# Optimization experiments

Measured on AMD Instinct MI355X. Metric: run time of the kernel, lower is better.

## Reference

```python
import jax, jax.numpy as jnp
import numpy as np

FS = 20.832e6      # sampling rate [Hz]
FDEMOD = 5.208e6   # demodulation frequency [Hz]
C = 1540.0         # sound speed [m/s]
FNUM = 1.0
MIN_W = 1e-3
EPS = 1e-5         # BatchNorm eps
EVENT = 0
TWO_PI = 2.0 * np.pi


def _cba(x, w, b, g, beta, pad):
    # Conv2d (NCHW) + BatchNorm2d (training-mode batch stats, biased var) + ReLU
    y = jax.lax.conv_general_dilated(x, w, (1, 1), ((0, 0), (pad, pad)),
                                     dimension_numbers=('NCHW', 'OIHW', 'NCHW'))
    y = y + b[None, :, None, None]
    mu = jnp.mean(y, axis=(0, 2, 3), keepdims=True)
    var = jnp.mean((y - mu) ** 2, axis=(0, 2, 3), keepdims=True)
    y = (y - mu) * jax.lax.rsqrt(var + EPS) * g[None, :, None, None] + beta[None, :, None, None]
    return jax.nn.relu(y)


def _forward(idata, qdata, angles, ele_pos, time_zero, grid,
             conv_w1, conv_b1, bn_g1, bn_b1,
             conv_w2, conv_b2, bn_g2, bn_b2,
             conv_w3, conv_b3, bn_g3, bn_b3,
             conv_w4, conv_b4, bn_g4, bn_b4):
    # --- normalization of raw I/Q data ---
    nrm = jnp.max(jnp.sqrt(idata ** 2 + qdata ** 2))
    idat = idata / nrm
    qdat = qdata / nrm
    H, Wd = grid.shape[:2]
    pix = grid.reshape(-1, 3)                               # [P,3]
    E = ele_pos.shape[0]
    ns = idat.shape[-1]
    ang = angles[EVENT]
    # --- delays in samples: plane-wave tx delay + per-element rx focus delay ---
    txdel = (pix[:, 0] * jnp.sin(ang) + pix[:, 2] * jnp.cos(ang)
             + time_zero[EVENT] * C) * (FS / C)             # [P]
    rxdel = jnp.linalg.norm(pix[None, :, :] - ele_pos[:, None, :], axis=-1) * (FS / C)  # [E,P]
    delays = txdel[None, :] + rxdel                         # [E,P]
    # --- 1D linear interp with zero padding ---
    # (grid_sample(bilinear, align_corners=False) on a 1xN image with the
    #  coordinate mapping in the source is exactly sampling at `delays`)
    d0 = jnp.floor(delays)
    frac = delays - d0
    d0i = d0.astype(jnp.int32)

    def gather(sig, idx):  # sig [E,ns], idx [E,P]
        v = jnp.take_along_axis(sig, jnp.clip(idx, 0, ns - 1), axis=1)
        return jnp.where((idx >= 0) & (idx < ns), v, 0.0)

    isig, qsig = idat[EVENT], qdat[EVENT]                   # [E,ns]
    ifoc = gather(isig, d0i) * (1.0 - frac) + gather(isig, d0i + 1) * frac
    qfoc = gather(qsig, d0i) * (1.0 - frac) + gather(qsig, d0i + 1) * frac
    # --- complex demodulation rotation ---
    tshift = delays / FS - pix[None, :, 2] * 2.0 / C
    theta = TWO_PI * FDEMOD * tshift
    ct, st = jnp.cos(theta), jnp.sin(theta)
    ir = ifoc * ct - qfoc * st
    qr = qfoc * ct + ifoc * st
    # [1,H,W,E,2]  (== torch idas/qdas view + squeeze(-2))
    inputData = jnp.transpose(jnp.stack([ir, qr], axis=-1), (1, 0, 2)).reshape(H, Wd, E, 2)[None]
    # --- receive apodization (orthogonal f-number mask), [H,W,E] ---
    v = pix[None, :, :] - ele_pos[:, None, :]
    vx, vz = v[:, :, 0], v[:, :, 2]
    px = pix[None, :, 0]
    # |vz/vx| > fnum written division-free as |vz| > fnum*|vx| (equivalent since vz>0)
    mrx = ((jnp.abs(vz) > FNUM * jnp.abs(vx)) | (jnp.abs(vx) <= MIN_W)
           | ((vx >= MIN_W) & (px <= ele_pos[0, 0]))
           | ((vx <= -MIN_W) & (px >= ele_pos[-1, 0])))
    apod_rx = jnp.transpose(mrx.astype(jnp.float32).reshape(E, H, Wd), (1, 2, 0))
    # --- transmit apodization (plane-wave footprint), [H,W] ---
    x_proj = pix[:, 0] - pix[:, 2] * jnp.tan(ang)
    mtx = (x_proj >= ele_pos[0, 0] * 1.2) & (x_proj <= ele_pos[-1, 0] * 1.2)
    apod_tx = mtx.astype(jnp.float32).reshape(H, Wd)
    inputData = inputData * apod_rx[None, :, :, :, None] * apod_tx[None, :, :, None, None]
    # --- per-element weighting CNN over [1, 2, H*W, E] ---
    x = jnp.transpose(inputData, (0, 4, 3, 1, 2)).reshape(1, 2, E, H * Wd)
    x = jnp.swapaxes(x, 2, 3)                               # [1,2,HW,E]
    x = _cba(x, conv_w1, conv_b1, bn_g1, bn_b1, 32)
    x = _cba(x, conv_w2, conv_b2, bn_g2, bn_b2, 7)
    x = _cba(x, conv_w3, conv_b3, bn_g3, bn_b3, 7)
    x = _cba(x, conv_w4, conv_b4, bn_g4, bn_b4, 1)          # [1,1,HW,E]
    weights = jnp.swapaxes(x[:, 0], 1, 2).reshape(1, E, H, Wd)
    singleW = jnp.sum(weights, axis=1)                      # [1,H,W]
    comp = jnp.mean(inputData * singleW[:, :, :, None, None], axis=-2)  # [1,H,W,2]
    mag = jnp.sqrt(jnp.sum(comp ** 2, axis=-1))
    ydb = 20.0 * jnp.log10(mag + 1e-20)
    y = ydb[0]
    return y - jnp.max(y)


def setup_inputs():
    key = jax.random.key(0)
    ks = jax.random.split(key, 8)
    na, ne, ns = 16, 128, 2048
    H, Wd = 128, 256
    idata = jax.random.normal(ks[0], (na, ne, ns), jnp.float32)
    qdata = jax.random.normal(ks[1], (na, ne, ns), jnp.float32)
    angles = jnp.linspace(-0.1, 0.1, na, dtype=jnp.float32)
    ex = jnp.linspace(-19.05e-3, 19.05e-3, ne, dtype=jnp.float32)
    ele_pos = jnp.stack([ex, jnp.zeros(ne, jnp.float32), jnp.zeros(ne, jnp.float32)], axis=-1)
    time_zero = jnp.zeros((na,), jnp.float32)
    xg = jnp.linspace(-17e-3, 17e-3, H, dtype=jnp.float32)
    zg = jnp.linspace(5e-3, 55e-3, Wd, dtype=jnp.float32)
    gx, gz = jnp.meshgrid(xg, zg, indexing='ij')
    grid = jnp.stack([gx, jnp.zeros_like(gx), gz], axis=-1)

    def conv_init(k, o, i, kh, kw):
        return jax.random.normal(k, (o, i, kh, kw), jnp.float32) * (1.0 / np.sqrt(i * kh * kw))

    return dict(idata=idata, qdata=qdata, angles=angles, ele_pos=ele_pos,
                time_zero=time_zero, grid=grid,
                conv_w1=conv_init(ks[2], 8, 2, 1, 65), conv_b1=jnp.zeros(8, jnp.float32),
                bn_g1=jnp.ones(8, jnp.float32), bn_b1=jnp.zeros(8, jnp.float32),
                conv_w2=conv_init(ks[3], 8, 8, 1, 15), conv_b2=jnp.zeros(8, jnp.float32),
                bn_g2=jnp.ones(8, jnp.float32), bn_b2=jnp.zeros(8, jnp.float32),
                conv_w3=conv_init(ks[4], 8, 8, 1, 15), conv_b3=jnp.zeros(8, jnp.float32),
                bn_g3=jnp.ones(8, jnp.float32), bn_b3=jnp.zeros(8, jnp.float32),
                conv_w4=conv_init(ks[5], 1, 8, 1, 3), conv_b4=jnp.zeros(1, jnp.float32),
                bn_g4=jnp.ones(1, jnp.float32), bn_b4=jnp.zeros(1, jnp.float32))


def reference(idata, qdata, angles, ele_pos, time_zero, grid,
              conv_w1, conv_b1, bn_g1, bn_b1,
              conv_w2, conv_b2, bn_g2, bn_b2,
              conv_w3, conv_b3, bn_g3, bn_b3,
              conv_w4, conv_b4, bn_g4, bn_b4):
    return _forward(idata, qdata, angles, ele_pos, time_zero, grid,
                    conv_w1, conv_b1, bn_g1, bn_b1,
                    conv_w2, conv_b2, bn_g2, bn_b2,
                    conv_w3, conv_b3, bn_g3, bn_b3,
                    conv_w4, conv_b4, bn_g4, bn_b4)
```

## Files before the change

### kernel.cpp

```cpp
#include <hip/hip_runtime.h>
#include <hip/hip_bf16.h>


#define E_    128
#define NPIX  32768
#define NS_   (NPIX * E_)
#define NSAMP 2048

static constexpr double PI_D     = 3.14159265358979323846;
static constexpr double FS_D     = 20832000.0;
static constexpr double FDEMOD_D = 5208000.0;
static constexpr double C_D      = 1540.0;

typedef __attribute__((ext_vector_type(8))) short short8;
typedef __attribute__((ext_vector_type(4))) float f32x4;

union U8 { uint4 u4; unsigned u32[4]; unsigned short us[8]; short8 s8; };

__device__ __forceinline__ unsigned short f2bf(float f) {
  unsigned u = __float_as_uint(f);
  unsigned r = (u + 0x7fffu + ((u >> 16) & 1u)) >> 16;
  return (unsigned short)r;
}
__device__ __forceinline__ unsigned cvt_pk_bf16(float lo, float hi) {
  unsigned r;
  asm("v_cvt_pk_bf16_f32 %0, %1, %2" : "=v"(r) : "v"(lo), "v"(hi));
  return r;
}
__device__ __forceinline__ float bflo(unsigned w) { return __uint_as_float(w << 16); }
__device__ __forceinline__ float bfhi(unsigned w) { return __uint_as_float(w & 0xFFFF0000u); }
__device__ __forceinline__ float bf2f(unsigned short s) {
  return __uint_as_float((unsigned)s << 16);
}

__device__ __forceinline__ float wave_reduce_sum(float v) {
  #pragma unroll
  for (int off = 32; off; off >>= 1) v += __shfl_xor(v, off);
  return v;
}
__device__ __forceinline__ float wave_reduce_max(float v) {
  #pragma unroll
  for (int off = 32; off; off >>= 1) v = fmaxf(v, __shfl_xor(v, off));
  return v;
}

template <int NBLK>
__device__ __forceinline__ void stats8v(const float4* __restrict__ part4,
                                        const float* __restrict__ g,
                                        const float* __restrict__ beta,
                                        float* __restrict__ A,
                                        float* __restrict__ Bc) {
  __shared__ float red[4][16];
  __shared__ float sums[16];
  const int tid = threadIdx.x;
  constexpr int K = (NBLK * 4) / 256;
  float ax = 0.f, ay = 0.f, az = 0.f, aw = 0.f;
  #pragma unroll
  for (int k = 0; k < K; ++k) {
    const float4 q = part4[tid + k * 256];
    ax += q.x; ay += q.y; az += q.z; aw += q.w;
  }
  #pragma unroll
  for (int off = 4; off <= 32; off <<= 1) {
    ax += __shfl_xor(ax, off);
    ay += __shfl_xor(ay, off);
    az += __shfl_xor(az, off);
    aw += __shfl_xor(aw, off);
  }
  const int lane = tid & 63, wv = tid >> 6;
  if (lane < 4) {
    red[wv][lane * 4 + 0] = ax;
    red[wv][lane * 4 + 1] = ay;
    red[wv][lane * 4 + 2] = az;
    red[wv][lane * 4 + 3] = aw;
  }
  __syncthreads();
  if (tid < 16)
    sums[tid] = red[0][tid] + red[1][tid] + red[2][tid] + red[3][tid];
  __syncthreads();
  if (tid < 8) {
    const float s = sums[tid], ss = sums[tid + 8];
    const float count = (float)NS_;
    const float mu = s / count;
    const float var = fmaxf(ss / count - mu * mu, 0.f);
    const float Av = g[tid] * rsqrtf(var + 1e-5f);
    red[0][tid] = Av;
    red[1][tid] = beta[tid] - mu * Av;
  }
  __syncthreads();
  #pragma unroll
  for (int i = 0; i < 8; ++i) { A[i] = red[0][i]; Bc[i] = red[1][i]; }
}

__device__ __forceinline__ uint4 bn_unit(uint4 v, const float* A, const float* B) {
  U8 in; in.u4 = v;
  unsigned ow[4];
  #pragma unroll
  for (int w = 0; w < 4; ++w) {
    const unsigned wd = in.u32[w];
    const float yl = fmaxf(0.f, fmaf(A[2 * w], bflo(wd), B[2 * w]));
    const float yh = fmaxf(0.f, fmaf(A[2 * w + 1], bfhi(wd), B[2 * w + 1]));
    ow[w] = cvt_pk_bf16(yl, yh);
  }
  return make_uint4(ow[0], ow[1], ow[2], ow[3]);
}

__global__ __launch_bounds__(256) void k_init(const float4* __restrict__ id4,
                                              const float4* __restrict__ qd4,
                                              float* __restrict__ pmaxsq) {
  const int idx = blockIdx.x * 256 + threadIdx.x;
  const float4 iv = id4[idx];
  const float4 qv = qd4[idx];
  float m = fmaxf(fmaxf(iv.x * iv.x + qv.x * qv.x, iv.y * iv.y + qv.y * qv.y),
                  fmaxf(iv.z * iv.z + qv.z * qv.z, iv.w * iv.w + qv.w * qv.w));
  m = wave_reduce_max(m);
  __shared__ float sm[4];
  if ((threadIdx.x & 63) == 0) sm[threadIdx.x >> 6] = m;
  __syncthreads();
  if (threadIdx.x == 0)
    pmaxsq[blockIdx.x] = fmaxf(fmaxf(sm[0], sm[1]), fmaxf(sm[2], sm[3]));
}

__global__ __launch_bounds__(256) void k_beamform(
    const float4* __restrict__ id4, const float4* __restrict__ qd4,
    const float* __restrict__ angles, const float* __restrict__ ele_pos,
    const float* __restrict__ time_zero, const float* __restrict__ grid,
    const float* __restrict__ pmaxsq, unsigned* __restrict__ x0t) {
  __shared__ float2 sig[NSAMP];
  __shared__ float smax[4];
  const int e = blockIdx.x & 127;
  const int chunk = blockIdx.x >> 7;

  const float4* irow = id4 + e * (NSAMP / 4);
  const float4* qrow = qd4 + e * (NSAMP / 4);
  #pragma unroll
  for (int k0 = 0; k0 < 2; ++k0) {
    const int k = k0 * 256 + threadIdx.x;
    const float4 iv = irow[k];
    const float4 qv = qrow[k];
    sig[4 * k + 0] = make_float2(iv.x, qv.x);
    sig[4 * k + 1] = make_float2(iv.y, qv.y);
    sig[4 * k + 2] = make_float2(iv.z, qv.z);
    sig[4 * k + 3] = make_float2(iv.w, qv.w);
  }
  float mx = 0.f;
  for (int i = threadIdx.x; i < 4096; i += 256) mx = fmaxf(mx, pmaxsq[i]);
  mx = wave_reduce_max(mx);
  if ((threadIdx.x & 63) == 0) smax[threadIdx.x >> 6] = mx;
  __syncthreads();
  const float inv =
      1.0f / sqrtf(fmaxf(fmaxf(smax[0], smax[1]), fmaxf(smax[2], smax[3])));

  const float ang = angles[0];
  const float tz  = time_zero[0];

  constexpr float SC    = (float)(FS_D / C_D);
  constexpr float TH2R  = (float)(2.0 * FDEMOD_D / C_D);
  constexpr float TWOPI = (float)(2.0 * PI_D);

  const float sa = __sinf(ang);
  const float ca = __cosf(ang);
  const float ta = sa / ca;
  const float ex  = ele_pos[e * 3];
  const float ex0 = ele_pos[0];
  const float exl = ele_pos[127 * 3];

  #pragma unroll
  for (int s = 0; s < 4; ++s) {
    const int p = chunk * 1024 + s * 256 + threadIdx.x;
    const float px = grid[p * 3 + 0];
    const float pz = grid[p * 3 + 2];

    const float txdel = (px * sa + pz * ca + tz * (float)C_D) * SC;
    const float dx = px - ex;
    const float rxdel = sqrtf(dx * dx + pz * pz) * SC;

    const float delays = txdel + rxdel;
    const float d0 = floorf(delays);
    const float frac = delays - d0;
    const int i0 = (int)d0;

    const int c0 = min(max(i0, 0), NSAMP - 1);
    const int c1 = min(max(i0 + 1, 0), NSAMP - 1);
    const float2 s0 = sig[c0];
    const float2 s1 = sig[c1];
    const bool m0 = (i0 >= 0) && (i0 < NSAMP);
    const bool m1 = (i0 + 1 >= 0) && (i0 + 1 < NSAMP);
    const float iv0 = m0 ? s0.x : 0.f;
    const float qv0 = m0 ? s0.y : 0.f;
    const float iv1 = m1 ? s1.x : 0.f;
    const float qv1 = m1 ? s1.y : 0.f;
    const float ifoc = (iv0 * (1.f - frac) + iv1 * frac) * inv;
    const float qfoc = (qv0 * (1.f - frac) + qv1 * frac) * inv;

    const float trev = fmaf(delays, 0.25f, -pz * TH2R);
    const float fr = trev - floorf(trev);
    const float st = __sinf(fr * TWOPI);
    const float ct = __cosf(fr * TWOPI);
    const float ir = ifoc * ct - qfoc * st;
    const float qr = qfoc * ct + ifoc * st;

    const float avx = fabsf(dx);
    const bool mrx = (fabsf(pz) > avx) || (avx <= 0.001f) ||
                     ((dx >= 0.001f) && (px <= ex0)) ||
                     ((dx <= -0.001f) && (px >= exl));
    const float xproj = px - pz * ta;
    const bool mtx = (xproj >= ex0 * 1.2f) && (xproj <= exl * 1.2f);
    const float a = (mrx && mtx) ? 1.f : 0.f;

    x0t[(size_t)e * NPIX + p] = cvt_pk_bf16(ir * a, qr * a);
  }
}

#define CONV1_P 32
#define ROWW    213

__global__ __launch_bounds__(256, 4) void k_conv1(
    const unsigned* __restrict__ x0t, const float* __restrict__ wgt,
    const float* __restrict__ bias, uint2* __restrict__ outp,
    float* __restrict__ partial,
    float* __restrict__ sumI, float* __restrict__ sumQ) {
  __shared__ unsigned tile[CONV1_P * ROWW];
  const int tid = threadIdx.x;
  const int lane = tid & 63;
  const int wv = tid >> 6;
  const int n = lane & 15, kq = lane >> 4;
  const int p0 = blockIdx.x * CONV1_P;

  short8 af2[6];
  #pragma unroll
  for (int m = 0; m < 6; ++m) {
    U8 u;
    #pragma unroll
    for (int j = 0; j < 8; ++j) {
      const int oc = n & 7;
      const int mm = (n < 8) ? m : (m - 1);
      const int tap = mm * 16 + kq * 4 + (j >> 1);
      const int ic = j & 1;
      const float w = (mm >= 0 && tap < 65) ? wgt[(oc * 2 + ic) * 65 + tap] : 0.f;
      u.us[j] = f2bf(w);
    }
    af2[m] = u.s8;
  }
  float bias_r[4];
  #pragma unroll
  for (int r = 0; r < 4; ++r) bias_r[r] = bias[(kq & 1) * 4 + r];

  for (int i = tid; i < CONV1_P * 32; i += 256)
    tile[(i >> 5) * ROWW + (i & 31)] = 0u;
  for (int i = tid; i < CONV1_P * 64; i += 256) {
    const int c = i & 63;
    if (c < ROWW - 160) tile[(i >> 6) * ROWW + 160 + c] = 0u;
  }
  {
    const int lp = tid & 31;
    const int e0 = tid >> 5;
    #pragma unroll
    for (int i = 0; i < 16; ++i) {
      const int e = i * 8 + e0;
      tile[lp * ROWW + 32 + e] = x0t[(size_t)e * NPIX + p0 + lp];
    }
  }
  __syncthreads();

  float sum[4] = {0, 0, 0, 0}, ssq[4] = {0, 0, 0, 0};
  const int sbase = n + kq * 4;

  for (int j8 = 0; j8 < 8; ++j8) {
    const int lpx = wv * 8 + j8;
    const int p = p0 + lpx;
    const unsigned* row = tile + lpx * ROWW;
    uint2* orow = outp + (size_t)p * 256;

    {
      const unsigned v0 = row[32 + lane];
      const unsigned v1 = row[96 + lane];
      float si = bflo(v0) + bflo(v1);
      float sq = bfhi(v0) + bfhi(v1);
      si = wave_reduce_sum(si);
      sq = wave_reduce_sum(sq);
      if (lane == 0) { sumI[p] = si; sumQ[p] = sq; }
    }

    U8 win[12];
    #pragma unroll
    for (int q = 0; q < 12; ++q)
      #pragma unroll
      for (int c = 0; c < 4; ++c) win[q].u32[c] = row[sbase + 16 * q + c];

    #pragma unroll
    for (int pi = 0; pi < 4; ++pi) {
      f32x4 acc = {bias_r[0], bias_r[1], bias_r[2], bias_r[3]};
      #pragma unroll
      for (int m = 0; m < 6; ++m)
        acc = __builtin_amdgcn_mfma_f32_16x16x32_bf16(af2[m], win[2 * pi + m].s8,
                                                      acc, 0, 0, 0);
      const unsigned lo = cvt_pk_bf16(acc[0], acc[1]);
      const unsigned hi = cvt_pk_bf16(acc[2], acc[3]);
      orow[((2 * pi + (kq >> 1)) * 16 + n) * 2 + (kq & 1)] = make_uint2(lo, hi);
      #pragma unroll
      for (int r = 0; r < 4; ++r) { const float v = acc[r]; sum[r] += v; ssq[r] += v * v; }
    }
  }

  #pragma unroll
  for (int off = 1; off <= 8; off <<= 1)
    #pragma unroll
    for (int r = 0; r < 4; ++r) { sum[r] += __shfl_xor(sum[r], off); ssq[r] += __shfl_xor(ssq[r], off); }
  #pragma unroll
  for (int r = 0; r < 4; ++r) { sum[r] += __shfl_xor(sum[r], 32); ssq[r] += __shfl_xor(ssq[r], 32); }
  __shared__ float s_red[4][16];
  if (lane == 0)
    #pragma unroll
    for (int r = 0; r < 4; ++r) { s_red[wv][r] = sum[r]; s_red[wv][8 + r] = ssq[r]; }
  if (lane == 16)
    #pragma unroll
    for (int r = 0; r < 4; ++r) { s_red[wv][4 + r] = sum[r]; s_red[wv][12 + r] = ssq[r]; }
  __syncthreads();
  if (tid < 16)
    partial[blockIdx.x * 16 + tid] =
        s_red[0][tid] + s_red[1][tid] + s_red[2][tid] + s_red[3][tid];
}

template <int NBLK_IN>
__global__ __launch_bounds__(256) void k_conv23(
    const uint4* __restrict__ inp, const float* __restrict__ wgt,
    const float* __restrict__ bias,
    const float4* __restrict__ part_in,
    const float* __restrict__ g_in, const float* __restrict__ be_in,
    uint2* __restrict__ outp, float* __restrict__ partial) {
  __shared__ uint4 s_row[4][144];
  const int tid = threadIdx.x;
  const int lane = tid & 63;
  const int wv = tid >> 6;
  const int gw = blockIdx.x * 4 + wv;
  const int n = lane & 15, kq = lane >> 4;

  uint4 v0 = inp[(size_t)gw * 128 + lane];
  uint4 v1 = inp[(size_t)gw * 128 + 64 + lane];

  float A[8], Bc[8];
  stats8v<NBLK_IN>(part_in, g_in, be_in, A, Bc);

  short8 af[4];
  #pragma unroll
  for (int m = 0; m < 4; ++m) {
    U8 u;
    #pragma unroll
    for (int j = 0; j < 8; ++j) {
      const int tap = m * 4 + kq;
      const float w = (n < 8 && tap < 15) ? wgt[(n * 8 + j) * 15 + tap] : 0.f;
      u.us[j] = f2bf(w);
    }
    af[m] = u.s8;
  }
  float bias_r[4];
  #pragma unroll
  for (int r = 0; r < 4; ++r) {
    const int oo = kq * 4 + r;
    bias_r[r] = (oo < 8) ? bias[oo] : 0.f;
  }

  uint4* lds = s_row[wv];
  if (lane < 7)  lds[lane] = make_uint4(0, 0, 0, 0);
  if (lane >= 7 && lane < 16) lds[128 + lane] = make_uint4(0, 0, 0, 0);

  float sum[4] = {0, 0, 0, 0}, ssq[4] = {0, 0, 0, 0};

  #pragma unroll 1
  for (int it = 0; it < 4; ++it) {
    const int p = gw + it * 8192;
    lds[7 + lane]  = bn_unit(v0, A, Bc);
    lds[71 + lane] = bn_unit(v1, A, Bc);

    if (it < 3) {
      const uint4* ng = inp + (size_t)(p + 8192) * 128;
      v0 = ng[lane];
      v1 = ng[64 + lane];
    }

    uint2* orow = outp + (size_t)p * 256;
    for (int t = 0; t < 8; ++t) {
      f32x4 acc = {bias_r[0], bias_r[1], bias_r[2], bias_r[3]};
      const int base = t * 16 + n + kq;
      #pragma unroll
      for (int m = 0; m < 4; ++m) {
        U8 b;
        b.u4 = lds[base + m * 4];
        acc = __builtin_amdgcn_mfma_f32_16x16x32_bf16(af[m], b.s8, acc, 0, 0, 0);
      }
      if (lane < 32) {
        const unsigned lo = cvt_pk_bf16(acc[0], acc[1]);
        const unsigned hi = cvt_pk_bf16(acc[2], acc[3]);
        orow[(t * 16 + n) * 2 + kq] = make_uint2(lo, hi);
        #pragma unroll
        for (int r = 0; r < 4; ++r) { const float v = acc[r]; sum[r] += v; ssq[r] += v * v; }
      }
    }
  }

  #pragma unroll
  for (int off = 1; off <= 8; off <<= 1)
    #pragma unroll
    for (int r = 0; r < 4; ++r) { sum[r] += __shfl_xor(sum[r], off); ssq[r] += __shfl_xor(ssq[r], off); }
  __shared__ float s_red[4][16];
  if (lane == 0)
    #pragma unroll
    for (int r = 0; r < 4; ++r) { s_red[wv][r] = sum[r]; s_red[wv][8 + r] = ssq[r]; }
  if (lane == 16)
    #pragma unroll
    for (int r = 0; r < 4; ++r) { s_red[wv][4 + r] = sum[r]; s_red[wv][12 + r] = ssq[r]; }
  __syncthreads();
  if (tid < 16)
    partial[blockIdx.x * 16 + tid] =
        s_red[0][tid] + s_red[1][tid] + s_red[2][tid] + s_red[3][tid];
}

__global__ __launch_bounds__(256) void k_conv4(
    const uint4* __restrict__ inp,
    const float4* __restrict__ part_in,
    const float* __restrict__ g3, const float* __restrict__ be3,
    const float* __restrict__ w4, const float* __restrict__ b4,
    unsigned short* __restrict__ y4b, float* __restrict__ partial) {
  float A[8], Bc[8];
  stats8v<2048>(part_in, g3, be3, A, Bc);

  const float bb = b4[0];
  float w4r[24];
  #pragma unroll
  for (int i = 0; i < 24; ++i) w4r[i] = w4[i];

  float s = 0.f, ss = 0.f;
  #pragma unroll 1
  for (int it = 0; it < 8; ++it) {
    const int idx = blockIdx.x * 256 + threadIdx.x + it * 524288;
    const int p = idx >> 7, e = idx & 127;
    float acc = bb;
    const uint4* row = inp + (size_t)p * 128 + e;
    #pragma unroll
    for (int kt = 0; kt < 3; ++kt) {
      const int ee = e + kt - 1;
      if (ee >= 0 && ee < E_) {
        U8 u; u.u4 = row[kt - 1];
        #pragma unroll
        for (int i = 0; i < 8; ++i) {
          const unsigned wd = u.u32[i >> 1];
          const float x = (i & 1) ? bfhi(wd) : bflo(wd);
          const float v = fmaxf(0.f, fmaf(A[i], x, Bc[i]));
          acc = fmaf(w4r[i * 3 + kt], v, acc);
        }
      }
    }
    y4b[idx] = f2bf(acc);
    s += acc;
    ss += acc * acc;
  }

  s = wave_reduce_sum(s);
  ss = wave_reduce_sum(ss);
  __shared__ float sm[4][2];
  if ((threadIdx.x & 63) == 0) { sm[threadIdx.x >> 6][0] = s; sm[threadIdx.x >> 6][1] = ss; }
  __syncthreads();
  if (threadIdx.x == 0) {
    partial[blockIdx.x * 2 + 0] = sm[0][0] + sm[1][0] + sm[2][0] + sm[3][0];
    partial[blockIdx.x * 2 + 1] = sm[0][1] + sm[1][1] + sm[2][1] + sm[3][1];
  }
}

__global__ __launch_bounds__(256) void k_final(const float* __restrict__ sumI,
                                               const float* __restrict__ sumQ,
                                               const unsigned short* __restrict__ y4b,
                                               const float4* __restrict__ part_in,
                                               const float* __restrict__ g4,
                                               const float* __restrict__ be4,
                                               float* __restrict__ ydb,
                                               float* __restrict__ pmax) {
  __shared__ float sAB[2];
  {
    const int tid = threadIdx.x;
    float s = 0.f, ss = 0.f;
    #pragma unroll
    for (int k = 0; k < 4; ++k) {
      const float4 q = part_in[tid + k * 256];
      s += q.x + q.z;
      ss += q.y + q.w;
    }
    s = wave_reduce_sum(s);
    ss = wave_reduce_sum(ss);
    __shared__ float sm[4][2];
    if ((tid & 63) == 0) { sm[tid >> 6][0] = s; sm[tid >> 6][1] = ss; }
    __syncthreads();
    if (tid == 0) {
      s  = sm[0][0] + sm[1][0] + sm[2][0] + sm[3][0];
      ss = sm[0][1] + sm[1][1] + sm[2][1] + sm[3][1];
      const float count = (float)NS_;
      const float mu = s / count;
      const float var = fmaxf(ss / count - mu * mu, 0.f);
      const float Av = g4[0] * rsqrtf(var + 1e-5f);
      sAB[0] = Av;
      sAB[1] = be4[0] - mu * Av;
    }
    __syncthreads();
  }
  const float A = sAB[0], B = sAB[1];

  const int w = threadIdx.x >> 6;
  const int lane = threadIdx.x & 63;
  const int p = blockIdx.x * 4 + w;
  const size_t base = (size_t)p * E_;

  float sw = fmaxf(0.f, fmaf(A, bf2f(y4b[base + lane]), B)) +
             fmaxf(0.f, fmaf(A, bf2f(y4b[base + lane + 64]), B));
  sw = wave_reduce_sum(sw);

  __shared__ float s_m[4];
  if (lane == 0) {
    const float ci = sw * sumI[p] * (1.f / (float)E_);
    const float cq = sw * sumQ[p] * (1.f / (float)E_);
    const float mag = sqrtf(ci * ci + cq * cq);
    const float v = 20.f * log10f(mag + 1e-20f);
    ydb[p] = v;
    s_m[w] = v;
  }
  __syncthreads();
  if (threadIdx.x == 0)
    pmax[blockIdx.x] = fmaxf(fmaxf(s_m[0], s_m[1]), fmaxf(s_m[2], s_m[3]));
}

__global__ __launch_bounds__(256) void k_sub(const float* __restrict__ ydb,
                                             const float* __restrict__ pmax,
                                             float* __restrict__ out) {
  float m = -3.4e38f;
  for (int i = threadIdx.x; i < NPIX / 4; i += 256) m = fmaxf(m, pmax[i]);
  m = wave_reduce_max(m);
  __shared__ float sm[4];
  if ((threadIdx.x & 63) == 0) sm[threadIdx.x >> 6] = m;
  __syncthreads();
  __shared__ float sgm;
  if (threadIdx.x == 0)
    sgm = fmaxf(fmaxf(sm[0], sm[1]), fmaxf(sm[2], sm[3]));
  __syncthreads();
  const int i = blockIdx.x * 256 + threadIdx.x;
  out[i] = ydb[i] - sgm;
}

static constexpr size_t OFF_A     = 0;
static constexpr size_t OFF_Y4    = 0;
static constexpr size_t OFF_YDB   = 16777216;
static constexpr size_t OFF_PMAX  = 16908288;
static constexpr size_t OFF_BUF1  = 67108864;
static constexpr size_t OFF_SUMI  = 134217728;
static constexpr size_t OFF_SUMQ  = 134348800;
static constexpr size_t OFF_PART0 = 134479872;
static constexpr size_t OFF_PART1 = 134610944;
static constexpr size_t OFF_PMSQ  = 134742016;

extern "C" void kernel_launch(void* const* d_in, const int* in_sizes, int n_in,
                              void* d_out, int out_size, void* d_ws, size_t ws_size,
                              hipStream_t stream) {
  const float* idata     = (const float*)d_in[0];
  const float* qdata     = (const float*)d_in[1];
  const float* angles    = (const float*)d_in[2];
  const float* ele_pos   = (const float*)d_in[3];
  const float* time_zero = (const float*)d_in[4];
  const float* grid      = (const float*)d_in[5];
  const float* w1 = (const float*)d_in[6];  const float* b1 = (const float*)d_in[7];
  const float* g1 = (const float*)d_in[8];  const float* be1 = (const float*)d_in[9];
  const float* w2 = (const float*)d_in[10]; const float* b2 = (const float*)d_in[11];
  const float* g2 = (const float*)d_in[12]; const float* be2 = (const float*)d_in[13];
  const float* w3 = (const float*)d_in[14]; const float* b3 = (const float*)d_in[15];
  const float* g3 = (const float*)d_in[16]; const float* be3 = (const float*)d_in[17];
  const float* w4 = (const float*)d_in[18]; const float* b4 = (const float*)d_in[19];
  const float* g4 = (const float*)d_in[20]; const float* be4 = (const float*)d_in[21];

  char* ws = (char*)d_ws;
  unsigned*       x0t   = (unsigned*)(ws + OFF_A);
  uint4*          buf2  = (uint4*)(ws + OFF_A);
  unsigned short* y4b   = (unsigned short*)(ws + OFF_Y4);
  float*          ydb   = (float*)(ws + OFF_YDB);
  float*          pmax  = (float*)(ws + OFF_PMAX);
  uint4*          buf1  = (uint4*)(ws + OFF_BUF1);
  float*          sumI  = (float*)(ws + OFF_SUMI);
  float*          sumQ  = (float*)(ws + OFF_SUMQ);
  float*          part0 = (float*)(ws + OFF_PART0);
  float*          part1 = (float*)(ws + OFF_PART1);
  float*          pmsq  = (float*)(ws + OFF_PMSQ);

  k_init<<<4096, 256, 0, stream>>>((const float4*)idata, (const float4*)qdata, pmsq);
  k_beamform<<<4096, 256, 0, stream>>>((const float4*)idata, (const float4*)qdata,
                                       angles, ele_pos, time_zero, grid,
                                       pmsq, x0t);

  k_conv1<<<NPIX / CONV1_P, 256, 0, stream>>>(x0t, w1, b1, (uint2*)buf1, part0,
                                              sumI, sumQ);

  k_conv23<1024><<<2048, 256, 0, stream>>>(buf1, w2, b2, (const float4*)part0,
                                           g1, be1, (uint2*)buf2, part1);

  k_conv23<2048><<<2048, 256, 0, stream>>>(buf2, w3, b3, (const float4*)part1,
                                           g2, be2, (uint2*)buf1, part0);

  k_conv4<<<2048, 256, 0, stream>>>(buf1, (const float4*)part0, g3, be3,
                                    w4, b4, y4b, part1);

  k_final<<<NPIX / 4, 256, 0, stream>>>(sumI, sumQ, y4b, (const float4*)part1,
                                        g4, be4, ydb, pmax);
  k_sub<<<NPIX / 256, 256, 0, stream>>>(ydb, pmax, (float*)d_out);
}
```

Baseline: 266.8 us.

## Finalize BatchNorm stats in last-finishing block instead of every consumer block

Before, every block of each consumer kernel re-reduced all per-block partial sums to get BatchNorm scale and shift. Now the producer kernel uses an atomic counter with a threadfence so the last block to finish reduces the partials once and writes scale/shift to a small buffer. Consumer kernels just load 16 floats. This removes redundant reduction traffic and barriers in thousands of blocks, at the cost of a serial tail in one block plus atomics, and counters that must be reset each launch (done in k_init).

```diff
diff --git a/kernel.cpp b/kernel.cpp
--- a/kernel.cpp
+++ b/kernel.cpp
@@ -45,15 +45,22 @@
 }
 
 template <int NBLK>
-__device__ __forceinline__ void stats8v(const float4* __restrict__ part4,
-                                        const float* __restrict__ g,
-                                        const float* __restrict__ beta,
-                                        float* __restrict__ A,
-                                        float* __restrict__ Bc) {
-  __shared__ float red[4][16];
-  __shared__ float sums[16];
+__device__ __forceinline__ void bn_finalize_last(const float* __restrict__ partial,
+                                                 unsigned* __restrict__ cnt,
+                                                 const float* __restrict__ g,
+                                                 const float* __restrict__ beta,
+                                                 float* __restrict__ AB) {
+  __shared__ unsigned lastFlag;
+  __threadfence();
+  __syncthreads();
+  if (threadIdx.x == 0)
+    lastFlag = (atomicAdd(cnt, 1u) == (unsigned)(NBLK - 1)) ? 1u : 0u;
+  __syncthreads();
+  if (!lastFlag) return;
+
+  const float4* part4 = (const float4*)partial;
   const int tid = threadIdx.x;
-  constexpr int K = (NBLK * 4) / 256;
+  constexpr int K = (NBLK * 16) / (4 * 256);
   float ax = 0.f, ay = 0.f, az = 0.f, aw = 0.f;
   #pragma unroll
   for (int k = 0; k < K; ++k) {
@@ -62,34 +69,65 @@
   }
   #pragma unroll
   for (int off = 4; off <= 32; off <<= 1) {
-    ax += __shfl_xor(ax, off);
-    ay += __shfl_xor(ay, off);
-    az += __shfl_xor(az, off);
-    aw += __shfl_xor(aw, off);
-  }
+    ax += __shfl_xor(ax, off); ay += __shfl_xor(ay, off);
+    az += __shfl_xor(az, off); aw += __shfl_xor(aw, off);
+  }
+  __shared__ float red[4][16];
   const int lane = tid & 63, wv = tid >> 6;
   if (lane < 4) {
-    red[wv][lane * 4 + 0] = ax;
-    red[wv][lane * 4 + 1] = ay;
-    red[wv][lane * 4 + 2] = az;
-    red[wv][lane * 4 + 3] = aw;
-  }
-  __syncthreads();
-  if (tid < 16)
-    sums[tid] = red[0][tid] + red[1][tid] + red[2][tid] + red[3][tid];
+    red[wv][lane * 4 + 0] = ax; red[wv][lane * 4 + 1] = ay;
+    red[wv][lane * 4 + 2] = az; red[wv][lane * 4 + 3] = aw;
+  }
   __syncthreads();
   if (tid < 8) {
-    const float s = sums[tid], ss = sums[tid + 8];
+    const float s  = red[0][tid] + red[1][tid] + red[2][tid] + red[3][tid];
+    const float ss = red[0][tid + 8] + red[1][tid + 8] + red[2][tid + 8] + red[3][tid + 8];
     const float count = (float)NS_;
     const float mu = s / count;
     const float var = fmaxf(ss / count - mu * mu, 0.f);
     const float Av = g[tid] * rsqrtf(var + 1e-5f);
-    red[0][tid] = Av;
-    red[1][tid] = beta[tid] - mu * Av;
-  }
-  __syncthreads();
-  #pragma unroll
-  for (int i = 0; i < 8; ++i) { A[i] = red[0][i]; Bc[i] = red[1][i]; }
+    AB[2 * tid] = Av;
+    AB[2 * tid + 1] = beta[tid] - mu * Av;
+  }
+}
+
+__device__ __forceinline__ void bn1_finalize_last(const float* __restrict__ partial,
+                                                  unsigned* __restrict__ cnt,
+                                                  const float* __restrict__ g,
+                                                  const float* __restrict__ beta,
+                                                  float* __restrict__ AB) {
+  __shared__ unsigned lastFlag;
+  __threadfence();
+  __syncthreads();
+  if (threadIdx.x == 0)
+    lastFlag = (atomicAdd(cnt, 1u) == 2047u) ? 1u : 0u;
+  __syncthreads();
+  if (!lastFlag) return;
+
+  const int tid = threadIdx.x;
+  const float4* p4 = (const float4*)partial;
+  float s = 0.f, ss = 0.f;
+  #pragma unroll
+  for (int k = 0; k < 4; ++k) {
+    const float4 q = p4[tid + k * 256];
+    s += q.x + q.z;
+    ss += q.y + q.w;
+  }
+  s = wave_reduce_sum(s);
+  ss = wave_reduce_sum(ss);
+  __shared__ float sm[4][2];
+  if ((tid & 63) == 0) { sm[tid >> 6][0] = s; sm[tid >> 6][1] = ss; }
+  __syncthreads();
+  if (tid == 0) {
+    s  = sm[0][0] + sm[1][0] + sm[2][0] + sm[3][0];
+    ss = sm[0][1] + sm[1][1] + sm[2][1] + sm[3][1];
+    const float count = (float)NS_;
+    const float mu = s / count;
+    const float var = fmaxf(ss / count - mu * mu, 0.f);
+    const float Av = g[0] * rsqrtf(var + 1e-5f);
+    AB[0] = Av;
+    AB[1] = beta[0] - mu * Av;
+  }
 }
 
 __device__ __forceinline__ uint4 bn_unit(uint4 v, const float* A, const float* B) {
@@ -107,7 +145,9 @@
 
 __global__ __launch_bounds__(256) void k_init(const float4* __restrict__ id4,
                                               const float4* __restrict__ qd4,
-                                              float* __restrict__ pmaxsq) {
+                                              float* __restrict__ pmaxsq,
+                                              unsigned* __restrict__ cnt) {
+  if (blockIdx.x == 0 && threadIdx.x < 4) cnt[threadIdx.x] = 0u;
   const int idx = blockIdx.x * 256 + threadIdx.x;
   const float4 iv = id4[idx];
   const float4 qv = qd4[idx];
@@ -218,7 +258,9 @@
 __global__ __launch_bounds__(256, 4) void k_conv1(
     const unsigned* __restrict__ x0t, const float* __restrict__ wgt,
     const float* __restrict__ bias, uint2* __restrict__ outp,
-    float* __restrict__ partial,
+    float* __restrict__ partial, unsigned* __restrict__ cnt,
+    const float* __restrict__ g, const float* __restrict__ beta,
+    float* __restrict__ AB,
     float* __restrict__ sumI, float* __restrict__ sumQ) {
   __shared__ unsigned tile[CONV1_P * ROWW];
   const int tid = threadIdx.x;
@@ -320,15 +362,18 @@
   if (tid < 16)
     partial[blockIdx.x * 16 + tid] =
         s_red[0][tid] + s_red[1][tid] + s_red[2][tid] + s_red[3][tid];
-}
-
-template <int NBLK_IN>
+
+  bn_finalize_last<NPIX / CONV1_P>(partial, cnt, g, beta, AB);
+}
+
 __global__ __launch_bounds__(256) void k_conv23(
     const uint4* __restrict__ inp, const float* __restrict__ wgt,
     const float* __restrict__ bias,
-    const float4* __restrict__ part_in,
-    const float* __restrict__ g_in, const float* __restrict__ be_in,
-    uint2* __restrict__ outp, float* __restrict__ partial) {
+    const float* __restrict__ ABin,
+    uint2* __restrict__ outp, float* __restrict__ partial,
+    unsigned* __restrict__ cnt,
+    const float* __restrict__ g, const float* __restrict__ beta,
+    float* __restrict__ ABout) {
   __shared__ uint4 s_row[4][144];
   const int tid = threadIdx.x;
   const int lane = tid & 63;
@@ -340,7 +385,8 @@
   uint4 v1 = inp[(size_t)gw * 128 + 64 + lane];
 
   float A[8], Bc[8];
-  stats8v<NBLK_IN>(part_in, g_in, be_in, A, Bc);
+  #pragma unroll
+  for (int i = 0; i < 8; ++i) { A[i] = ABin[2 * i]; Bc[i] = ABin[2 * i + 1]; }
 
   short8 af[4];
   #pragma unroll
@@ -414,16 +460,21 @@
   if (tid < 16)
     partial[blockIdx.x * 16 + tid] =
         s_red[0][tid] + s_red[1][tid] + s_red[2][tid] + s_red[3][tid];
+
+  bn_finalize_last<2048>(partial, cnt, g, beta, ABout);
 }
 
 __global__ __launch_bounds__(256) void k_conv4(
     const uint4* __restrict__ inp,
-    const float4* __restrict__ part_in,
-    const float* __restrict__ g3, const float* __restrict__ be3,
+    const float* __restrict__ ABin,
     const float* __restrict__ w4, const float* __restrict__ b4,
-    unsigned short* __restrict__ y4b, float* __restrict__ partial) {
+    unsigned short* __restrict__ y4b, float* __restrict__ partial,
+    unsigned* __restrict__ cnt,
+    const float* __restrict__ g4, const float* __restrict__ be4,
+    float* __restrict__ AB4) {
   float A[8], Bc[8];
-  stats8v<2048>(part_in, g3, be3, A, Bc);
+  #pragma unroll
+  for (int i = 0; i < 8; ++i) { A[i] = ABin[2 * i]; Bc[i] = ABin[2 * i + 1]; }
 
   const float bb = b4[0];
   float w4r[24];
@@ -465,44 +516,17 @@
     partial[blockIdx.x * 2 + 0] = sm[0][0] + sm[1][0] + sm[2][0] + sm[3][0];
     partial[blockIdx.x * 2 + 1] = sm[0][1] + sm[1][1] + sm[2][1] + sm[3][1];
   }
+
+  bn1_finalize_last(partial, cnt, g4, be4, AB4);
 }
 
 __global__ __launch_bounds__(256) void k_final(const float* __restrict__ sumI,
                                                const float* __restrict__ sumQ,
                                                const unsigned short* __restrict__ y4b,
-                                               const float4* __restrict__ part_in,
-                                               const float* __restrict__ g4,
-                                               const float* __restrict__ be4,
+                                               const float* __restrict__ AB4,
                                                float* __restrict__ ydb,
                                                float* __restrict__ pmax) {
-  __shared__ float sAB[2];
-  {
-    const int tid = threadIdx.x;
-    float s = 0.f, ss = 0.f;
-    #pragma unroll
-    for (int k = 0; k < 4; ++k) {
-      const float4 q = part_in[tid + k * 256];
-      s += q.x + q.z;
-      ss += q.y + q.w;
-    }
-    s = wave_reduce_sum(s);
-    ss = wave_reduce_sum(ss);
-    __shared__ float sm[4][2];
-    if ((tid & 63) == 0) { sm[tid >> 6][0] = s; sm[tid >> 6][1] = ss; }
-    __syncthreads();
-    if (tid == 0) {
-      s  = sm[0][0] + sm[1][0] + sm[2][0] + sm[3][0];
-      ss = sm[0][1] + sm[1][1] + sm[2][1] + sm[3][1];
-      const float count = (float)NS_;
-      const float mu = s / count;
-      const float var = fmaxf(ss / count - mu * mu, 0.f);
-      const float Av = g4[0] * rsqrtf(var + 1e-5f);
-      sAB[0] = Av;
-      sAB[1] = be4[0] - mu * Av;
-    }
-    __syncthreads();
-  }
-  const float A = sAB[0], B = sAB[1];
+  const float A = AB4[0], B = AB4[1];
 
   const int w = threadIdx.x >> 6;
   const int lane = threadIdx.x & 63;
@@ -554,6 +578,8 @@
 static constexpr size_t OFF_PART0 = 134479872;
 static constexpr size_t OFF_PART1 = 134610944;
 static constexpr size_t OFF_PMSQ  = 134742016;
+static constexpr size_t OFF_AB    = 134758400;
+static constexpr size_t OFF_CNT   = 134758656;
 
 extern "C" void kernel_launch(void* const* d_in, const int* in_sizes, int n_in,
                               void* d_out, int out_size, void* d_ws, size_t ws_size,
@@ -585,25 +611,28 @@
   float*          part0 = (float*)(ws + OFF_PART0);
   float*          part1 = (float*)(ws + OFF_PART1);
   float*          pmsq  = (float*)(ws + OFF_PMSQ);
-
-  k_init<<<4096, 256, 0, stream>>>((const float4*)idata, (const float4*)qdata, pmsq);
+  float*          AB    = (float*)(ws + OFF_AB);
+  unsigned*       cnt   = (unsigned*)(ws + OFF_CNT);
+
+  k_init<<<4096, 256, 0, stream>>>((const float4*)idata, (const float4*)qdata,
+                                   pmsq, cnt);
   k_beamform<<<4096, 256, 0, stream>>>((const float4*)idata, (const float4*)qdata,
                                        angles, ele_pos, time_zero, grid,
                                        pmsq, x0t);
 
   k_conv1<<<NPIX / CONV1_P, 256, 0, stream>>>(x0t, w1, b1, (uint2*)buf1, part0,
+                                              cnt + 0, g1, be1, AB + 0,
                                               sumI, sumQ);
 
-  k_conv23<1024><<<2048, 256, 0, stream>>>(buf1, w2, b2, (const float4*)part0,
-                                           g1, be1, (uint2*)buf2, part1);
-
-  k_conv23<2048><<<2048, 256, 0, stream>>>(buf2, w3, b3, (const float4*)part1,
-                                           g2, be2, (uint2*)buf1, part0);
-
-  k_conv4<<<2048, 256, 0, stream>>>(buf1, (const float4*)part0, g3, be3,
-                                    w4, b4, y4b, part1);
-
-  k_final<<<NPIX / 4, 256, 0, stream>>>(sumI, sumQ, y4b, (const float4*)part1,
-                                        g4, be4, ydb, pmax);
+  k_conv23<<<2048, 256, 0, stream>>>(buf1, w2, b2, AB + 0, (uint2*)buf2, part1,
+                                     cnt + 1, g2, be2, AB + 16);
+
+  k_conv23<<<2048, 256, 0, stream>>>(buf2, w3, b3, AB + 16, (uint2*)buf1, part0,
+                                     cnt + 2, g3, be3, AB + 32);
+
+  k_conv4<<<2048, 256, 0, stream>>>(buf1, AB + 32, w4, b4, y4b, part1,
+                                    cnt + 3, g4, be4, AB + 48);
+
+  k_final<<<NPIX / 4, 256, 0, stream>>>(sumI, sumQ, y4b, AB + 48, ydb, pmax);
   k_sub<<<NPIX / 256, 256, 0, stream>>>(ydb, pmax, (float*)d_out);
 }
```

Result: slower. 987.6 us (+270.2%).
